# Optimization experiments

Hardware: AMD Instinct MI355X
Metric: run time of the kernel (lower is better)

Reference implementation:

```python
import jax, jax.numpy as jnp
import numpy as np

ALPHA = 1.0
INF = 1e4  # larger than any possible distance in a 256x256 image


def _row_dist_to_zero(x):
    """1D distance along last axis to nearest zero pixel. x: [..., W] (0/1)."""
    W = x.shape[-1]
    idx = jnp.arange(W, dtype=jnp.float32)
    is0 = x == 0
    # nearest zero at-or-before each position
    last0 = jax.lax.cummax(jnp.where(is0, idx, -1.0), axis=x.ndim - 1)
    fwd = jnp.where(last0 >= 0, idx - last0, INF)
    # nearest zero at-or-after each position (suffix max of -idx)
    neg_next0 = jax.lax.cummax(jnp.where(is0, -idx, -INF), axis=x.ndim - 1, reverse=True)
    bwd = jnp.where(neg_next0 > -INF, (-neg_next0) - idx, INF)
    return jnp.minimum(fwd, bwd)


def _edt_2d(target):
    """Exact Euclidean distance transform per [B,C] map: distance from nonzero
    pixels to nearest zero pixel (matches scipy.ndimage.distance_transform_edt)."""
    B, C, H, W = target.shape
    g = _row_dist_to_zero(target)            # [B,C,H,W] distance along width
    g2 = g * g
    i = jnp.arange(H, dtype=jnp.float32)
    dk2 = (i[:, None] - i[None, :]) ** 2     # [H(out), H(k)]
    # dt2[b,c,i,w] = min_k g2[b,c,k,w] + (i-k)^2
    d2 = jnp.min(g2[:, :, None, :, :] + dk2[None, None, :, :, None], axis=3)
    return jnp.sqrt(d2)


def _distance_map(target):
    dist = _edt_2d(target)
    dmax = jnp.max(dist, axis=(-2, -1), keepdims=True)
    return dist / (dmax + 1e-7)


def setup_inputs() -> dict:
    key = jax.random.key(0)
    k1, k2 = jax.random.split(key)
    pred = jax.random.normal(k1, (8, 1, 256, 256), dtype=jnp.float32)
    target = jax.random.randint(k2, (8, 1, 256, 256), 0, 2).astype(jnp.float32)
    return {"pred": pred, "target": target}


def reference(pred, target):
    dist_map = _distance_map(target)
    weight_map = 1.0 + ALPHA * dist_map
    # numerically stable BCE with logits, reduction='none'
    bce = jnp.maximum(pred, 0.0) - pred * target + jnp.log1p(jnp.exp(-jnp.abs(pred)))
    return jnp.mean(weight_map * bce)
```

## Files before the change

kernel.cpp:

```cpp
#include <hip/hip_runtime.h>
#include <math.h>

#define BATCH 8
#define H 256
#define W 256
#define NPIX (BATCH * H * W)
#define NBLK2 512

__device__ __forceinline__ float bce_logits(float p, float t) {
    return fmaxf(p, 0.0f) - p * t + log1pf(expf(-fabsf(p)));
}

__global__ void __launch_bounds__(256) row_edt4(const float* __restrict__ target,
                                                float4* __restrict__ gi4) {
    __shared__ unsigned long long mlds[4][4];
    const int tid = threadIdx.x;
    const int v = tid >> 6, l = tid & 63;
    const float* imgr = target + (size_t)blockIdx.x * 4 * W;

    #pragma unroll
    for (int j = 0; j < 4; ++j) {
        float t = imgr[j * W + tid];
        unsigned long long m = __ballot(t == 0.0f);
        if (l == 0) mlds[j][v] = m;
    }
    __syncthreads();

    const int p = tid;
    float g[4];
    #pragma unroll
    for (int j = 0; j < 4; ++j) {
        unsigned long long mw[4] = {mlds[j][0], mlds[j][1], mlds[j][2], mlds[j][3]};
        int best = 1 << 20;
        #pragma unroll
        for (int w = 0; w < 4; ++w) {
            const int rel = p - (w << 6);
            const unsigned long long m = mw[w];
            unsigned long long mlo = (rel < 0)  ? 0ull
                                   : (rel >= 63) ? m : (m & ((2ull << rel) - 1ull));
            unsigned long long mhi = (rel <= 0) ? m
                                   : (rel > 63)  ? 0ull : (m & (~0ull << rel));
            if (mlo) best = min(best, rel - (63 - __builtin_clzll(mlo)));
            if (mhi) best = min(best, __builtin_ctzll(mhi) - rel);
        }
        float d = (best > 255) ? 1e4f : (float)best;
        g[j] = d * d;
    }
    gi4[(size_t)blockIdx.x * 256 + tid] = make_float4(g[0], g[1], g[2], g[3]);
}

__global__ void __launch_bounds__(256) envelope_bce(
        const float4* __restrict__ gi4, const float* __restrict__ pred,
        const float* __restrict__ target,
        float* __restrict__ pmx, float* __restrict__ psb, float* __restrict__ psdb) {
    __shared__ float red[3][4];
    const int tid = threadIdx.x;
    const int wv = tid >> 6, l = tid & 63;
    const int b  = blockIdx.x >> 6;
    const int cs = (blockIdx.x >> 4) & 3;
    const int rs = blockIdx.x & 15;
    const int c  = (cs << 6) + l;
    const int i0 = (rs << 4) + (wv << 2);

    const float4* gp = gi4 + (size_t)b * 64 * 256 + c;

    float acc0 = 3.0e38f, acc1 = 3.0e38f, acc2 = 3.0e38f, acc3 = 3.0e38f;
    float d0 = (float)i0, d1 = d0 + 1.0f, d2 = d0 + 2.0f, d3 = d0 + 3.0f;
    #pragma unroll 4
    for (int k4 = 0; k4 < 64; ++k4) {
        float4 g = gp[(size_t)k4 * 256];
        float e0, e1, e2, e3;
        e0 = d0; e1 = d1; e2 = d2; e3 = d3;
        acc0 = fminf(acc0, fminf(fmaf(e0, e0, g.x), fmaf(e0 - 1.0f, e0 - 1.0f, g.y)));
        acc1 = fminf(acc1, fminf(fmaf(e1, e1, g.x), fmaf(e1 - 1.0f, e1 - 1.0f, g.y)));
        acc2 = fminf(acc2, fminf(fmaf(e2, e2, g.x), fmaf(e2 - 1.0f, e2 - 1.0f, g.y)));
        acc3 = fminf(acc3, fminf(fmaf(e3, e3, g.x), fmaf(e3 - 1.0f, e3 - 1.0f, g.y)));
        e0 -= 2.0f; e1 -= 2.0f; e2 -= 2.0f; e3 -= 2.0f;
        acc0 = fminf(acc0, fminf(fmaf(e0, e0, g.z), fmaf(e0 - 1.0f, e0 - 1.0f, g.w)));
        acc1 = fminf(acc1, fminf(fmaf(e1, e1, g.z), fmaf(e1 - 1.0f, e1 - 1.0f, g.w)));
        acc2 = fminf(acc2, fminf(fmaf(e2, e2, g.z), fmaf(e2 - 1.0f, e2 - 1.0f, g.w)));
        acc3 = fminf(acc3, fminf(fmaf(e3, e3, g.z), fmaf(e3 - 1.0f, e3 - 1.0f, g.w)));
        d0 -= 4.0f; d1 -= 4.0f; d2 -= 4.0f; d3 -= 4.0f;
    }

    const float* pp = pred   + ((size_t)(b * H + i0)) * W + c;
    const float* tp = target + ((size_t)(b * H + i0)) * W + c;
    float p0 = pp[0], p1 = pp[W], p2 = pp[2 * W], p3 = pp[3 * W];
    float t0 = tp[0], t1 = tp[W], t2 = tp[2 * W], t3 = tp[3 * W];

    float mx = fmaxf(fmaxf(acc0, acc1), fmaxf(acc2, acc3));
    float b0 = bce_logits(p0, t0), b1 = bce_logits(p1, t1);
    float b2 = bce_logits(p2, t2), b3 = bce_logits(p3, t3);
    float sb  = (b0 + b1) + (b2 + b3);
    float sdb = (sqrtf(acc0) * b0 + sqrtf(acc1) * b1)
              + (sqrtf(acc2) * b2 + sqrtf(acc3) * b3);

    #pragma unroll
    for (int o = 32; o > 0; o >>= 1) {
        mx  = fmaxf(mx, __shfl_down(mx, o, 64));
        sb  += __shfl_down(sb, o, 64);
        sdb += __shfl_down(sdb, o, 64);
    }
    if (l == 0) { red[0][wv] = mx; red[1][wv] = sb; red[2][wv] = sdb; }
    __syncthreads();
    if (tid == 0) {
        pmx [blockIdx.x] = fmaxf(fmaxf(red[0][0], red[0][1]), fmaxf(red[0][2], red[0][3]));
        psb [blockIdx.x] = (red[1][0] + red[1][1]) + (red[1][2] + red[1][3]);
        psdb[blockIdx.x] = (red[2][0] + red[2][1]) + (red[2][2] + red[2][3]);
    }
}

__global__ void final_reduce(const float* __restrict__ pmx, const float* __restrict__ psb,
                             const float* __restrict__ psdb, float* __restrict__ out) {
    const int tid = threadIdx.x;
    const int img = tid >> 5, j = tid & 31;
    const int e0 = (img << 6) + j, e1 = e0 + 32;
    float mx  = fmaxf(pmx[e0], pmx[e1]);
    float sb  = psb[e0] + psb[e1];
    float sdb = psdb[e0] + psdb[e1];
    #pragma unroll
    for (int o = 16; o > 0; o >>= 1) {
        mx  = fmaxf(mx, __shfl_down(mx, o, 32));
        sb  += __shfl_down(sb, o, 32);
        sdb += __shfl_down(sdb, o, 32);
    }
    __shared__ float cimg[8], simg[8];
    if (j == 0) {
        cimg[img] = sdb / (sqrtf(mx) + 1e-7f);
        simg[img] = sb;
    }
    __syncthreads();
    if (tid == 0) {
        float tot = 0.0f;
        #pragma unroll
        for (int i = 0; i < 8; ++i) tot += simg[i] + cimg[i];
        out[0] = tot * (1.0f / (float)NPIX);
    }
}

extern "C" void kernel_launch(void* const* d_in, const int* in_sizes, int n_in,
                              void* d_out, int out_size, void* d_ws, size_t ws_size,
                              hipStream_t stream) {
    const float* pred   = (const float*)d_in[0];
    const float* target = (const float*)d_in[1];

    float4* gi4 = (float4*)d_ws;
    float* pmx  = (float*)((char*)d_ws + (size_t)BATCH * 64 * 256 * sizeof(float4));
    float* psb  = pmx + NBLK2;
    float* psdb = psb + NBLK2;

    row_edt4<<<BATCH * 64, 256, 0, stream>>>(target, gi4);
    envelope_bce<<<NBLK2, 256, 0, stream>>>(gi4, pred, target, pmx, psb, psdb);
    final_reduce<<<1, 256, 0, stream>>>(pmx, psb, psdb, (float*)d_out);
}
```

Baseline: 75.57 us.

## Double envelope grid and fold final reduction into last-block atomic pass

The envelope kernel now runs twice as many blocks, each thread handling two output rows instead of four, to raise occupancy and parallelism on the column-min pass. The separate final_reduce launch is removed: a global counter, reset in the row kernel, lets the last finishing block do the cross-block reduction. This saves one kernel launch, but each thread gets less reuse of every loaded column of gi4, so total load traffic doubles.

```diff
diff --git a/kernel.cpp b/kernel.cpp
--- a/kernel.cpp
+++ b/kernel.cpp
@@ -5,14 +5,16 @@
 #define H 256
 #define W 256
 #define NPIX (BATCH * H * W)
-#define NBLK2 512
+#define NBLK2 1024
 
 __device__ __forceinline__ float bce_logits(float p, float t) {
     return fmaxf(p, 0.0f) - p * t + log1pf(expf(-fabsf(p)));
 }
 
 __global__ void __launch_bounds__(256) row_edt4(const float* __restrict__ target,
-                                                float4* __restrict__ gi4) {
+                                                float4* __restrict__ gi4,
+                                                unsigned int* __restrict__ counter) {
+    if (blockIdx.x == 0 && threadIdx.x == 0) *counter = 0u;
     __shared__ unsigned long long mlds[4][4];
     const int tid = threadIdx.x;
     const int v = tid >> 6, l = tid & 63;
@@ -52,48 +54,42 @@
 __global__ void __launch_bounds__(256) envelope_bce(
         const float4* __restrict__ gi4, const float* __restrict__ pred,
         const float* __restrict__ target,
-        float* __restrict__ pmx, float* __restrict__ psb, float* __restrict__ psdb) {
+        float* __restrict__ pmx, float* __restrict__ psb, float* __restrict__ psdb,
+        unsigned int* __restrict__ counter, float* __restrict__ out) {
     __shared__ float red[3][4];
+    __shared__ unsigned int lastFlag;
     const int tid = threadIdx.x;
     const int wv = tid >> 6, l = tid & 63;
-    const int b  = blockIdx.x >> 6;
-    const int cs = (blockIdx.x >> 4) & 3;
-    const int rs = blockIdx.x & 15;
+    const int b  = blockIdx.x >> 7;
+    const int cs = (blockIdx.x >> 5) & 3;
+    const int rs = blockIdx.x & 31;
     const int c  = (cs << 6) + l;
-    const int i0 = (rs << 4) + (wv << 2);
+    const int i0 = (rs << 3) + (wv << 1);
 
     const float4* gp = gi4 + (size_t)b * 64 * 256 + c;
 
-    float acc0 = 3.0e38f, acc1 = 3.0e38f, acc2 = 3.0e38f, acc3 = 3.0e38f;
-    float d0 = (float)i0, d1 = d0 + 1.0f, d2 = d0 + 2.0f, d3 = d0 + 3.0f;
-    #pragma unroll 4
+    float acc0 = 3.0e38f, acc1 = 3.0e38f;
+    float d = (float)i0;
+    #pragma unroll 8
     for (int k4 = 0; k4 < 64; ++k4) {
         float4 g = gp[(size_t)k4 * 256];
-        float e0, e1, e2, e3;
-        e0 = d0; e1 = d1; e2 = d2; e3 = d3;
-        acc0 = fminf(acc0, fminf(fmaf(e0, e0, g.x), fmaf(e0 - 1.0f, e0 - 1.0f, g.y)));
-        acc1 = fminf(acc1, fminf(fmaf(e1, e1, g.x), fmaf(e1 - 1.0f, e1 - 1.0f, g.y)));
-        acc2 = fminf(acc2, fminf(fmaf(e2, e2, g.x), fmaf(e2 - 1.0f, e2 - 1.0f, g.y)));
-        acc3 = fminf(acc3, fminf(fmaf(e3, e3, g.x), fmaf(e3 - 1.0f, e3 - 1.0f, g.y)));
-        e0 -= 2.0f; e1 -= 2.0f; e2 -= 2.0f; e3 -= 2.0f;
-        acc0 = fminf(acc0, fminf(fmaf(e0, e0, g.z), fmaf(e0 - 1.0f, e0 - 1.0f, g.w)));
-        acc1 = fminf(acc1, fminf(fmaf(e1, e1, g.z), fmaf(e1 - 1.0f, e1 - 1.0f, g.w)));
-        acc2 = fminf(acc2, fminf(fmaf(e2, e2, g.z), fmaf(e2 - 1.0f, e2 - 1.0f, g.w)));
-        acc3 = fminf(acc3, fminf(fmaf(e3, e3, g.z), fmaf(e3 - 1.0f, e3 - 1.0f, g.w)));
-        d0 -= 4.0f; d1 -= 4.0f; d2 -= 4.0f; d3 -= 4.0f;
+        float e = d;
+        acc0 = fminf(acc0, fminf(fmaf(e, e, g.x), fmaf(e - 1.0f, e - 1.0f, g.y)));
+        acc0 = fminf(acc0, fminf(fmaf(e - 2.0f, e - 2.0f, g.z), fmaf(e - 3.0f, e - 3.0f, g.w)));
+        float f = d + 1.0f;
+        acc1 = fminf(acc1, fminf(fmaf(f, f, g.x), fmaf(f - 1.0f, f - 1.0f, g.y)));
+        acc1 = fminf(acc1, fminf(fmaf(f - 2.0f, f - 2.0f, g.z), fmaf(f - 3.0f, f - 3.0f, g.w)));
+        d -= 4.0f;
     }
 
-    const float* pp = pred   + ((size_t)(b * H + i0)) * W + c;
-    const float* tp = target + ((size_t)(b * H + i0)) * W + c;
-    float p0 = pp[0], p1 = pp[W], p2 = pp[2 * W], p3 = pp[3 * W];
-    float t0 = tp[0], t1 = tp[W], t2 = tp[2 * W], t3 = tp[3 * W];
+    const size_t po = ((size_t)(b * H + i0)) * W + c;
+    float p0 = pred[po], p1 = pred[po + W];
+    float t0 = target[po], t1 = target[po + W];
 
-    float mx = fmaxf(fmaxf(acc0, acc1), fmaxf(acc2, acc3));
+    float mx = fmaxf(acc0, acc1);
     float b0 = bce_logits(p0, t0), b1 = bce_logits(p1, t1);
-    float b2 = bce_logits(p2, t2), b3 = bce_logits(p3, t3);
-    float sb  = (b0 + b1) + (b2 + b3);
-    float sdb = (sqrtf(acc0) * b0 + sqrtf(acc1) * b1)
-              + (sqrtf(acc2) * b2 + sqrtf(acc3) * b3);
+    float sb  = b0 + b1;
+    float sdb = sqrtf(acc0) * b0 + sqrtf(acc1) * b1;
 
     #pragma unroll
     for (int o = 32; o > 0; o >>= 1) {
@@ -107,34 +103,41 @@
         pmx [blockIdx.x] = fmaxf(fmaxf(red[0][0], red[0][1]), fmaxf(red[0][2], red[0][3]));
         psb [blockIdx.x] = (red[1][0] + red[1][1]) + (red[1][2] + red[1][3]);
         psdb[blockIdx.x] = (red[2][0] + red[2][1]) + (red[2][2] + red[2][3]);
-    }
-}
-
-__global__ void final_reduce(const float* __restrict__ pmx, const float* __restrict__ psb,
-                             const float* __restrict__ psdb, float* __restrict__ out) {
-    const int tid = threadIdx.x;
-    const int img = tid >> 5, j = tid & 31;
-    const int e0 = (img << 6) + j, e1 = e0 + 32;
-    float mx  = fmaxf(pmx[e0], pmx[e1]);
-    float sb  = psb[e0] + psb[e1];
-    float sdb = psdb[e0] + psdb[e1];
-    #pragma unroll
-    for (int o = 16; o > 0; o >>= 1) {
-        mx  = fmaxf(mx, __shfl_down(mx, o, 32));
-        sb  += __shfl_down(sb, o, 32);
-        sdb += __shfl_down(sdb, o, 32);
-    }
-    __shared__ float cimg[8], simg[8];
-    if (j == 0) {
-        cimg[img] = sdb / (sqrtf(mx) + 1e-7f);
-        simg[img] = sb;
+        __threadfence();
+        unsigned int t = atomicAdd(counter, 1u);
+        lastFlag = (t == NBLK2 - 1) ? 1u : 0u;
     }
     __syncthreads();
-    if (tid == 0) {
-        float tot = 0.0f;
+
+    if (lastFlag) {
+        __threadfence();
+        const int img = tid >> 5, j = tid & 31;
+        float fmx = 0.0f, fsb = 0.0f, fsdb = 0.0f;
         #pragma unroll
-        for (int i = 0; i < 8; ++i) tot += simg[i] + cimg[i];
-        out[0] = tot * (1.0f / (float)NPIX);
+        for (int q = 0; q < 4; ++q) {
+            const int e = (img << 7) + j + (q << 5);
+            fmx  = fmaxf(fmx, pmx[e]);
+            fsb  += psb[e];
+            fsdb += psdb[e];
+        }
+        #pragma unroll
+        for (int o = 16; o > 0; o >>= 1) {
+            fmx  = fmaxf(fmx, __shfl_down(fmx, o, 32));
+            fsb  += __shfl_down(fsb, o, 32);
+            fsdb += __shfl_down(fsdb, o, 32);
+        }
+        __shared__ float cimg[8], simg[8];
+        if (j == 0) {
+            cimg[img] = fsdb / (sqrtf(fmx) + 1e-7f);
+            simg[img] = fsb;
+        }
+        __syncthreads();
+        if (tid == 0) {
+            float tot = 0.0f;
+            #pragma unroll
+            for (int i = 0; i < 8; ++i) tot += simg[i] + cimg[i];
+            out[0] = tot * (1.0f / (float)NPIX);
+        }
     }
 }
 
@@ -148,8 +151,9 @@
     float* pmx  = (float*)((char*)d_ws + (size_t)BATCH * 64 * 256 * sizeof(float4));
     float* psb  = pmx + NBLK2;
     float* psdb = psb + NBLK2;
+    unsigned int* counter = (unsigned int*)(psdb + NBLK2);
 
-    row_edt4<<<BATCH * 64, 256, 0, stream>>>(target, gi4);
-    envelope_bce<<<NBLK2, 256, 0, stream>>>(gi4, pred, target, pmx, psb, psdb);
-    final_reduce<<<1, 256, 0, stream>>>(pmx, psb, psdb, (float*)d_out);
+    row_edt4<<<BATCH * 64, 256, 0, stream>>>(target, gi4, counter);
+    envelope_bce<<<NBLK2, 256, 0, stream>>>(gi4, pred, target, pmx, psb, psdb,
+                                            counter, (float*)d_out);
 }
```

Measured after the change: 96.49 us. +27.7%, slower.

## Prune column envelope search with early-exit bidirectional scan

Applied to the files above, without the earlier changes.

Replaces the full 256-row min-plus scan per column with a scan that walks outward from the output rows and stops once the squared row offset exceeds every current minimum across the wavefront. The row distance buffer changes from a 4-row interleaved float4 layout to a plain row-major float layout to support the scattered row accesses. This removes most of the ALU and memory traffic of the vertical pass when distances are small, at the cost of data-dependent loop control and scalar loads.

```diff
diff --git a/kernel.cpp b/kernel.cpp
--- a/kernel.cpp
+++ b/kernel.cpp
@@ -11,8 +11,8 @@
     return fmaxf(p, 0.0f) - p * t + log1pf(expf(-fabsf(p)));
 }
 
-__global__ void __launch_bounds__(256) row_edt4(const float* __restrict__ target,
-                                                float4* __restrict__ gi4) {
+__global__ void __launch_bounds__(256) row_edt(const float* __restrict__ target,
+                                               float* __restrict__ g2) {
     __shared__ unsigned long long mlds[4][4];
     const int tid = threadIdx.x;
     const int v = tid >> 6, l = tid & 63;
@@ -27,7 +27,6 @@
     __syncthreads();
 
     const int p = tid;
-    float g[4];
     #pragma unroll
     for (int j = 0; j < 4; ++j) {
         unsigned long long mw[4] = {mlds[j][0], mlds[j][1], mlds[j][2], mlds[j][3]};
@@ -44,13 +43,12 @@
             if (mhi) best = min(best, __builtin_ctzll(mhi) - rel);
         }
         float d = (best > 255) ? 1e4f : (float)best;
-        g[j] = d * d;
+        g2[(size_t)blockIdx.x * 4 * W + j * W + tid] = d * d;
     }
-    gi4[(size_t)blockIdx.x * 256 + tid] = make_float4(g[0], g[1], g[2], g[3]);
 }
 
 __global__ void __launch_bounds__(256) envelope_bce(
-        const float4* __restrict__ gi4, const float* __restrict__ pred,
+        const float* __restrict__ g2, const float* __restrict__ pred,
         const float* __restrict__ target,
         float* __restrict__ pmx, float* __restrict__ psb, float* __restrict__ psdb) {
     __shared__ float red[3][4];
@@ -62,31 +60,40 @@
     const int c  = (cs << 6) + l;
     const int i0 = (rs << 4) + (wv << 2);
 
-    const float4* gp = gi4 + (size_t)b * 64 * 256 + c;
-
-    float acc0 = 3.0e38f, acc1 = 3.0e38f, acc2 = 3.0e38f, acc3 = 3.0e38f;
-    float d0 = (float)i0, d1 = d0 + 1.0f, d2 = d0 + 2.0f, d3 = d0 + 3.0f;
-    #pragma unroll 4
-    for (int k4 = 0; k4 < 64; ++k4) {
-        float4 g = gp[(size_t)k4 * 256];
-        float e0, e1, e2, e3;
-        e0 = d0; e1 = d1; e2 = d2; e3 = d3;
-        acc0 = fminf(acc0, fminf(fmaf(e0, e0, g.x), fmaf(e0 - 1.0f, e0 - 1.0f, g.y)));
-        acc1 = fminf(acc1, fminf(fmaf(e1, e1, g.x), fmaf(e1 - 1.0f, e1 - 1.0f, g.y)));
-        acc2 = fminf(acc2, fminf(fmaf(e2, e2, g.x), fmaf(e2 - 1.0f, e2 - 1.0f, g.y)));
-        acc3 = fminf(acc3, fminf(fmaf(e3, e3, g.x), fmaf(e3 - 1.0f, e3 - 1.0f, g.y)));
-        e0 -= 2.0f; e1 -= 2.0f; e2 -= 2.0f; e3 -= 2.0f;
-        acc0 = fminf(acc0, fminf(fmaf(e0, e0, g.z), fmaf(e0 - 1.0f, e0 - 1.0f, g.w)));
-        acc1 = fminf(acc1, fminf(fmaf(e1, e1, g.z), fmaf(e1 - 1.0f, e1 - 1.0f, g.w)));
-        acc2 = fminf(acc2, fminf(fmaf(e2, e2, g.z), fmaf(e2 - 1.0f, e2 - 1.0f, g.w)));
-        acc3 = fminf(acc3, fminf(fmaf(e3, e3, g.z), fmaf(e3 - 1.0f, e3 - 1.0f, g.w)));
-        d0 -= 4.0f; d1 -= 4.0f; d2 -= 4.0f; d3 -= 4.0f;
-    }
-
     const float* pp = pred   + ((size_t)(b * H + i0)) * W + c;
     const float* tp = target + ((size_t)(b * H + i0)) * W + c;
     float p0 = pp[0], p1 = pp[W], p2 = pp[2 * W], p3 = pp[3 * W];
     float t0 = tp[0], t1 = tp[W], t2 = tp[2 * W], t3 = tp[3 * W];
+
+    const float* gcol = g2 + (size_t)b * H * W + c;
+
+    float acc0 = 3.0e38f, acc1 = 3.0e38f, acc2 = 3.0e38f, acc3 = 3.0e38f;
+    int kd = i0 + 1, ku = i0 + 2;
+    float fd0 = (float)(i0 - kd), fu0 = (float)(ku - i0);
+    for (;;) {
+        if (kd >= 0) {
+            float g = gcol[(size_t)kd * W];
+            acc0 = fminf(acc0, fmaf(fd0, fd0, g));
+            float fd1 = fd0 + 1.0f, fd2 = fd0 + 2.0f, fd3 = fd0 + 3.0f;
+            acc1 = fminf(acc1, fmaf(fd1, fd1, g));
+            acc2 = fminf(acc2, fmaf(fd2, fd2, g));
+            acc3 = fminf(acc3, fmaf(fd3, fd3, g));
+        }
+        if (ku <= 255) {
+            float g = gcol[(size_t)ku * W];
+            float fu1 = fu0 - 1.0f, fu2 = fu0 - 2.0f, fu3 = fu0 - 3.0f;
+            acc0 = fminf(acc0, fmaf(fu0, fu0, g));
+            acc1 = fminf(acc1, fmaf(fu1, fu1, g));
+            acc2 = fminf(acc2, fmaf(fu2, fu2, g));
+            acc3 = fminf(acc3, fmaf(fu3, fu3, g));
+        }
+        --kd; ++ku; fd0 += 1.0f; fu0 += 1.0f;
+        float maxacc = fmaxf(fmaxf(acc0, acc1), fmaxf(acc2, acc3));
+        float dn = (float)(i0 - kd);
+        float up = (float)(ku - (i0 + 3));
+        bool alive = (kd >= 0 && dn * dn <= maxacc) || (ku <= 255 && up * up <= maxacc);
+        if (!__any(alive)) break;
+    }
 
     float mx = fmaxf(fmaxf(acc0, acc1), fmaxf(acc2, acc3));
     float b0 = bce_logits(p0, t0), b1 = bce_logits(p1, t1);
@@ -144,12 +151,12 @@
     const float* pred   = (const float*)d_in[0];
     const float* target = (const float*)d_in[1];
 
-    float4* gi4 = (float4*)d_ws;
-    float* pmx  = (float*)((char*)d_ws + (size_t)BATCH * 64 * 256 * sizeof(float4));
+    float* g2   = (float*)d_ws;
+    float* pmx  = (float*)((char*)d_ws + (size_t)NPIX * sizeof(float));
     float* psb  = pmx + NBLK2;
     float* psdb = psb + NBLK2;
 
-    row_edt4<<<BATCH * 64, 256, 0, stream>>>(target, gi4);
-    envelope_bce<<<NBLK2, 256, 0, stream>>>(gi4, pred, target, pmx, psb, psdb);
+    row_edt<<<BATCH * 64, 256, 0, stream>>>(target, g2);
+    envelope_bce<<<NBLK2, 256, 0, stream>>>(g2, pred, target, pmx, psb, psdb);
     final_reduce<<<1, 256, 0, stream>>>(pmx, psb, psdb, (float*)d_out);
 }
```

Result: faster. 67.38 us (-10.8%).
